# Performance work log

Measured on AMD Instinct MI355X. Metric: run time of the kernel, lower is better.

The kernel has to match this reference:

```python
import jax, jax.numpy as jnp
import numpy as np

C = 1024            # hidden_dim // compression_rate
IN_DIM = 1024
OUT_DIM = 1024
FFT_LEN = C // 2 + 1
CURV = 1e-4         # self.c
EPS = 1e-7
LN_EPS = 1e-5


def _mobius_scalar_mul(r, x, c):
    # r (x) x = tanh(r * atanh(sqrt(c)||x||)) * x / (sqrt(c)||x||)
    sqrt_c = jnp.sqrt(c)
    norm = jnp.maximum(jnp.linalg.norm(x, axis=-1, keepdims=True), EPS)
    scn = jnp.clip(sqrt_c * norm, EPS, 1.0 - 1e-5)
    return jnp.tanh(r * jnp.arctanh(scn)) * x / (sqrt_c * norm)


def _mobius_add(x, y, c):
    x2 = jnp.sum(x * x, axis=-1, keepdims=True)
    y2 = jnp.sum(y * y, axis=-1, keepdims=True)
    xy = jnp.sum(x * y, axis=-1, keepdims=True)
    num = (1.0 + 2.0 * c * xy + c * y2) * x + (1.0 - c * x2) * y
    den = 1.0 + 2.0 * c * xy + (c * c) * x2 * y2
    return num / jnp.maximum(den, EPS)


def _poincare_ball_layer(u, v, c, t):
    # geodesic-style interpolation: ((1-t) (x) u) (+) (t (x) v)
    return _mobius_add(_mobius_scalar_mul(1.0 - t, u, c),
                       _mobius_scalar_mul(t, v, c), c)


def setup_inputs() -> dict:
    key = jax.random.key(0)
    k_x, k_p, k_d = jax.random.split(key, 3)
    std = 0.02
    x = jax.random.normal(k_x, (4, 2048, IN_DIM), dtype=jnp.float32)
    proj_w = jax.random.normal(k_p, (C, IN_DIM), dtype=jnp.float32) * std
    freq_w = jnp.zeros((FFT_LEN,), dtype=jnp.float32)
    t = jnp.float32(0.3)
    ln_g = jnp.ones((C,), dtype=jnp.float32)
    ln_b = jnp.zeros((C,), dtype=jnp.float32)
    down_w = jax.random.normal(k_d, (OUT_DIM, C), dtype=jnp.float32) * std
    scale = jnp.float32(1.0)
    return {"x": x, "proj_w": proj_w, "ln_g": ln_g, "ln_b": ln_b,
            "freq_w": freq_w, "t": t, "down_w": down_w, "scale": scale}


def reference(x, proj_w, ln_g, ln_b, freq_w, t, down_w, scale):
    B, L, _ = x.shape
    # non-sep branch (hidden_dim > in_dim): silu(Linear(x))
    comp = jax.nn.silu(jnp.einsum('bli,ci->blc', x, proj_w))
    mu = jnp.mean(comp, axis=-1, keepdims=True)
    var = jnp.var(comp, axis=-1, keepdims=True)
    comp = (comp - mu) * jax.lax.rsqrt(var + LN_EPS) * ln_g + ln_b
    comp = comp.reshape(-1, C)                     # [B*L, C]
    Xf = jnp.fft.rfft(comp, axis=1)                # [B*L, C//2+1]
    w = jax.nn.softmax(freq_w)[None, :]
    flat = jnp.fft.irfft(Xf * w, n=C, axis=1)
    flat = jnp.nan_to_num(flat)
    shift = jnp.nan_to_num(t * flat)
    hyp = jnp.nan_to_num(_poincare_ball_layer(flat, shift, CURV, t))
    hyp = hyp.reshape(B, L, C)
    return jnp.einsum('blc,oc->blo', hyp, down_w) * scale
```

## Files before the change

### kernel.cpp

```cpp
#include <hip/hip_runtime.h>
#include <math.h>

typedef float f32x4 __attribute__((ext_vector_type(4)));
typedef __bf16 bf16x8 __attribute__((ext_vector_type(8)));

__device__ __forceinline__ unsigned short f2bf(float f) {
  unsigned u = __float_as_uint(f);
  unsigned r = (u + 0x7fffu + ((u >> 16) & 1u)) >> 16;
  return (unsigned short)r;
}
__device__ __forceinline__ float bf2f(unsigned short h) {
  return __uint_as_float(((unsigned)h) << 16);
}

__device__ __forceinline__ float blk_sum(float v, float* red, int tid) {
  #pragma unroll
  for (int o = 32; o; o >>= 1) v += __shfl_down(v, o);
  __syncthreads();
  if ((tid & 63) == 0) red[tid >> 6] = v;
  __syncthreads();
  return red[0] + red[1] + red[2] + red[3];
}

__global__ __launch_bounds__(256) void k_s(const float* __restrict__ fw,
                                           float* __restrict__ s) {
  __shared__ float wsh[513];
  __shared__ float red[4];
  int tid = threadIdx.x;
  float m = -1e30f;
  for (int i = tid; i < 513; i += 256) m = fmaxf(m, fw[i]);
  #pragma unroll
  for (int o = 32; o; o >>= 1) m = fmaxf(m, __shfl_down(m, o));
  if ((tid & 63) == 0) red[tid >> 6] = m;
  __syncthreads();
  m = fmaxf(fmaxf(red[0], red[1]), fmaxf(red[2], red[3]));
  float sum = 0.f;
  for (int i = tid; i < 513; i += 256) {
    float e = expf(fw[i] - m);
    wsh[i] = e;
    sum += e;
  }
  sum = blk_sum(sum, red, tid);
  float inv = 1.f / sum;

  int gid = blockIdx.x * 256 + tid;
  int d = gid >> 3;
  int chunk = gid & 7;
  float acc = 0.f;
  for (int f = 1 + chunk; f < 512; f += 8) {
    int p = (f * d) & 1023;
    acc += wsh[f] * __cosf(6.283185307179586f * (float)p * (1.f / 1024.f));
  }
  acc += __shfl_xor(acc, 1);
  acc += __shfl_xor(acc, 2);
  acc += __shfl_xor(acc, 4);
  if (chunk == 0) {
    float tot = wsh[0] + ((d & 1) ? -wsh[512] : wsh[512]) + 2.f * acc;
    s[d] = tot * inv * (1.f / 1024.f);
  }
}

__global__ __launch_bounds__(256) void k_prep(const float* __restrict__ x,
                                              const float* __restrict__ pw,
                                              const float* __restrict__ dw,
                                              const float* __restrict__ s,
                                              const float* __restrict__ ln_g,
                                              const float* __restrict__ ln_b,
                                              unsigned short* __restrict__ xb,
                                              unsigned short* __restrict__ pwb,
                                              unsigned short* __restrict__ dwb,
                                              unsigned short* __restrict__ Sg,
                                              float* __restrict__ Gs,
                                              float* __restrict__ Bs2) {
  __shared__ float red[4];
  int b = blockIdx.x;
  int tid = threadIdx.x;
  if (b < 8192) {
    int i = b * 256 + tid;
    float4 v = ((const float4*)x)[i];
    ushort4 o;
    o.x = f2bf(v.x); o.y = f2bf(v.y); o.z = f2bf(v.z); o.w = f2bf(v.w);
    ((ushort4*)xb)[i] = o;
  } else if (b < 9216) {
    int i = (b - 8192) * 256 + tid;
    float4 v = ((const float4*)pw)[i];
    ushort4 o;
    o.x = f2bf(v.x); o.y = f2bf(v.y); o.z = f2bf(v.z); o.w = f2bf(v.w);
    ((ushort4*)pwb)[i] = o;
  } else if (b < 10240) {
    int i = (b - 9216) * 256 + tid;
    float4 v = ((const float4*)dw)[i];
    ushort4 o;
    o.x = f2bf(v.x); o.y = f2bf(v.y); o.z = f2bf(v.z); o.w = f2bf(v.w);
    ((ushort4*)dwb)[i] = o;
  } else if (b < 11264) {
    int idx = (b - 10240) * 256 + tid;
    int n = idx >> 8;
    int k0 = (idx & 255) * 4;
    float4 gv = ((const float4*)ln_g)[idx & 255];
    ushort4 o;
    o.x = f2bf(gv.x * s[(k0 + 0 - n) & 1023]);
    o.y = f2bf(gv.y * s[(k0 + 1 - n) & 1023]);
    o.z = f2bf(gv.z * s[(k0 + 2 - n) & 1023]);
    o.w = f2bf(gv.w * s[(k0 + 3 - n) & 1023]);
    ((ushort4*)Sg)[idx] = o;
  } else {
    int n = b - 11264;
    int k0 = tid * 4;
    float4 gv = ((const float4*)ln_g)[tid];
    float4 bv = ((const float4*)ln_b)[tid];
    float s0 = s[(k0 + 0 - n) & 1023], s1 = s[(k0 + 1 - n) & 1023];
    float s2 = s[(k0 + 2 - n) & 1023], s3 = s[(k0 + 3 - n) & 1023];
    float gp = gv.x * s0 + gv.y * s1 + gv.z * s2 + gv.w * s3;
    float bp = bv.x * s0 + bv.y * s1 + bv.z * s2 + bv.w * s3;
    gp = blk_sum(gp, red, tid);
    bp = blk_sum(bp, red, tid);
    if (tid == 0) { Gs[n] = gp; Bs2[n] = bp; }
  }
}

__device__ __forceinline__ void gemm_body(const unsigned short* __restrict__ A,
                                          const unsigned short* __restrict__ B,
                                          int bm, int bn, int tid,
                                          char* AsB, char* BsB,
                                          f32x4 acc[4][4]) {
  const int lane = tid & 63;
  const int wave = tid >> 6;
  const int mhalf = (wave & 1) * 64;
  const int nhalf = (wave >> 1) * 64;
  const int ar = tid >> 3;
  const int ac = (((tid & 7) ^ (ar & 7))) * 8;
  const unsigned short* Abase = A + (size_t)(bm + ar) * 1024 + ac;
  const unsigned short* Bbase = B + (size_t)(bn + ar) * 1024 + ac;
  const int mrow = lane & 15;
  const int kq = lane >> 4;
  const int sw = mrow & 7;

  for (int kt = 0; kt < 16; ++kt) {
    const int k0 = kt * 64;
    #pragma unroll
    for (int r = 0; r < 4; ++r) {
      __builtin_amdgcn_global_load_lds(
          (const __attribute__((address_space(1))) void*)(Abase + (size_t)(r * 32) * 1024 + k0),
          (__attribute__((address_space(3))) void*)(AsB + r * 4096 + wave * 1024), 16, 0, 0);
      __builtin_amdgcn_global_load_lds(
          (const __attribute__((address_space(1))) void*)(Bbase + (size_t)(r * 32) * 1024 + k0),
          (__attribute__((address_space(3))) void*)(BsB + r * 4096 + wave * 1024), 16, 0, 0);
    }
    __syncthreads();
    #pragma unroll
    for (int kc = 0; kc < 2; ++kc) {
      const int chunk = (kc << 2) | kq;
      bf16x8 af[4], bfr[4];
      #pragma unroll
      for (int mt = 0; mt < 4; ++mt)
        af[mt] = *(const bf16x8*)(AsB + (mhalf + mt * 16 + mrow) * 128 + ((chunk ^ sw) << 4));
      #pragma unroll
      for (int nt = 0; nt < 4; ++nt)
        bfr[nt] = *(const bf16x8*)(BsB + (nhalf + nt * 16 + mrow) * 128 + ((chunk ^ sw) << 4));
      #pragma unroll
      for (int mt = 0; mt < 4; ++mt)
        #pragma unroll
        for (int nt = 0; nt < 4; ++nt)
          acc[mt][nt] = __builtin_amdgcn_mfma_f32_16x16x32_bf16(af[mt], bfr[nt], acc[mt][nt], 0, 0, 0);
    }
    __syncthreads();
  }
}

__global__ __launch_bounds__(256) void k_gemm1w2(const unsigned short* __restrict__ xb,
                                                 const unsigned short* __restrict__ pwb,
                                                 const unsigned short* __restrict__ dwb,
                                                 const unsigned short* __restrict__ Sg,
                                                 const float* __restrict__ ln_g,
                                                 const float* __restrict__ ln_b,
                                                 unsigned short* __restrict__ comp,
                                                 unsigned short* __restrict__ W2g,
                                                 float* __restrict__ rowsum,
                                                 float* __restrict__ rowsum2,
                                                 float* __restrict__ Gw,
                                                 float* __restrict__ Bw) {
  __shared__ __align__(16) unsigned short As[128 * 64];
  __shared__ __align__(16) unsigned short Bs[128 * 64];
  const int tid = threadIdx.x;
  const int lane = tid & 63;
  const int wave = tid >> 6;

  if (blockIdx.x < 256) {
    const unsigned short* Sc2 = Sg + (size_t)1024 * 1024;
    const int bm = ((int)blockIdx.x >> 4) * 64;
    const int bn = ((int)blockIdx.x & 15) * 64;
    const int wm = wave & 1;
    const int wn = wave >> 1;
    f32x4 acc[2][2] = {};
    const int ar = tid >> 3;
    const int ac = (((tid & 7) ^ (ar & 7))) * 8;
    const unsigned short* Abase = dwb + (size_t)(bm + ar) * 1024 + ac;
    const unsigned short* Bbase = Sc2 + (size_t)(bn + ar) * 1024 + ac;
    char* AsB = (char*)As;
    char* BsB = (char*)Bs;
    const int mrow = lane & 15;
    const int kq = lane >> 4;
    const int sw = mrow & 7;
    for (int kt = 0; kt < 16; ++kt) {
      const int k0 = kt * 64;
      #pragma unroll
      for (int r = 0; r < 2; ++r) {
        __builtin_amdgcn_global_load_lds(
            (const __attribute__((address_space(1))) void*)(Abase + (size_t)(r * 32) * 1024 + k0),
            (__attribute__((address_space(3))) void*)(AsB + r * 4096 + wave * 1024), 16, 0, 0);
        __builtin_amdgcn_global_load_lds(
            (const __attribute__((address_space(1))) void*)(Bbase + (size_t)(r * 32) * 1024 + k0),
            (__attribute__((address_space(3))) void*)(BsB + r * 4096 + wave * 1024), 16, 0, 0);
      }
      __syncthreads();
      #pragma unroll
      for (int kc = 0; kc < 2; ++kc) {
        const int chunk = (kc << 2) | kq;
        bf16x8 af[2], bfr[2];
        #pragma unroll
        for (int mt = 0; mt < 2; ++mt)
          af[mt] = *(const bf16x8*)(AsB + (wm * 32 + mt * 16 + mrow) * 128 + ((chunk ^ sw) << 4));
        #pragma unroll
        for (int nt = 0; nt < 2; ++nt)
          bfr[nt] = *(const bf16x8*)(BsB + (wn * 32 + nt * 16 + mrow) * 128 + ((chunk ^ sw) << 4));
        #pragma unroll
        for (int mt = 0; mt < 2; ++mt)
          #pragma unroll
          for (int nt = 0; nt < 2; ++nt)
            acc[mt][nt] = __builtin_amdgcn_mfma_f32_16x16x32_bf16(af[mt], bfr[nt], acc[mt][nt], 0, 0, 0);
      }
      __syncthreads();
    }
    const int col = bn + wn * 32 + (lane & 15);
    const int rbase = bm + wm * 32 + (lane >> 4) * 4;
    float gc[2], bc[2];
    #pragma unroll
    for (int nt = 0; nt < 2; ++nt) { gc[nt] = ln_g[col + nt * 16]; bc[nt] = ln_b[col + nt * 16]; }
    #pragma unroll
    for (int mt = 0; mt < 2; ++mt)
      #pragma unroll
      for (int r = 0; r < 4; ++r) {
        int row = rbase + mt * 16 + r;
        float gwp = 0.f, bwp = 0.f;
        #pragma unroll
        for (int nt = 0; nt < 2; ++nt) {
          float v = acc[mt][nt][r];
          W2g[(size_t)row * 1024 + (col + nt * 16)] = f2bf(gc[nt] * v);
          gwp += gc[nt] * v;
          bwp += bc[nt] * v;
        }
        gwp += __shfl_xor(gwp, 1); gwp += __shfl_xor(gwp, 2);
        gwp += __shfl_xor(gwp, 4); gwp += __shfl_xor(gwp, 8);
        bwp += __shfl_xor(bwp, 1); bwp += __shfl_xor(bwp, 2);
        bwp += __shfl_xor(bwp, 4); bwp += __shfl_xor(bwp, 8);
        if ((lane & 15) == 0) {
          atomicAdd(&Gw[row], gwp);
          atomicAdd(&Bw[row], bwp);
        }
      }
    return;
  }

  const int gid = blockIdx.x - 256;
  const int xcd = gid & 7;
  const int j = gid >> 3;
  const int ntile = j & 7;
  const int bmIdx = xcd + 8 * (j >> 3);
  const int bm = bmIdx * 128;
  const int bn = ntile * 128;
  f32x4 acc[4][4] = {};
  gemm_body(xb, pwb, bm, bn, tid, (char*)As, (char*)Bs, acc);

  const int col = bn + (wave >> 1) * 64 + (lane & 15);
  const int rbase = bm + (wave & 1) * 64 + (lane >> 4) * 4;
  #pragma unroll
  for (int mt = 0; mt < 4; ++mt)
    #pragma unroll
    for (int r = 0; r < 4; ++r) {
      const int row = rbase + mt * 16 + r;
      float s1 = 0.f, s2 = 0.f;
      #pragma unroll
      for (int nt = 0; nt < 4; ++nt) {
        float v = acc[mt][nt][r];
        float sv = v / (1.f + expf(-v));
        comp[(size_t)row * 1024 + (col + nt * 16)] = f2bf(sv);
        s1 += sv;
        s2 += sv * sv;
      }
      s1 += __shfl_xor(s1, 1); s1 += __shfl_xor(s1, 2);
      s1 += __shfl_xor(s1, 4); s1 += __shfl_xor(s1, 8);
      s2 += __shfl_xor(s2, 1); s2 += __shfl_xor(s2, 2);
      s2 += __shfl_xor(s2, 4); s2 += __shfl_xor(s2, 8);
      if ((lane & 15) == 0) {
        atomicAdd(&rowsum[row], s1);
        atomicAdd(&rowsum2[row], s2);
      }
    }
}

__device__ __forceinline__ float gamma_from_u2(float U2, float tv) {
  const float sc = 0.01f;
  const float c = 1e-4f;
  float nrm = sqrtf(U2);
  float nu = fmaxf(nrm, 1e-7f);
  float su = fminf(fmaxf(sc * nu, 1e-7f), 1.f - 1e-5f);
  float Af = tanhf((1.f - tv) * atanhf(su)) / (sc * nu);
  float nvn = fmaxf(fabsf(tv) * nrm, 1e-7f);
  float svv = fminf(fmaxf(sc * nvn, 1e-7f), 1.f - 1e-5f);
  float Bf = tv * tanhf(tv * atanhf(svv)) / (sc * nvn);
  float x2s = Af * Af * U2, y2s = Bf * Bf * U2, xys = Af * Bf * U2;
  float numc = (1.f + 2.f * c * xys + c * y2s) * Af + (1.f - c * x2s) * Bf;
  float den = fmaxf(1.f + 2.f * c * xys + c * c * x2s * y2s, 1e-7f);
  return numc / den;
}

__global__ __launch_bounds__(256) void k_gemm23(const unsigned short* __restrict__ comp,
                                                const unsigned short* __restrict__ Sg,
                                                const unsigned short* __restrict__ W2g,
                                                const float* __restrict__ rowsum,
                                                const float* __restrict__ rowsum2,
                                                const float* __restrict__ Gs,
                                                const float* __restrict__ Bs2,
                                                const float* __restrict__ Gw,
                                                const float* __restrict__ Bw,
                                                unsigned short* __restrict__ raw,
                                                float* __restrict__ u2) {
  __shared__ __align__(16) unsigned short As[128 * 64];
  __shared__ __align__(16) unsigned short Bs[128 * 64];
  __shared__ float muS[128], invS[128], GcS[128], BcS[128];
  const int tid = threadIdx.x;
  const int lane = tid & 63;
  const int wave = tid >> 6;
  const int xcd = blockIdx.x & 7;
  const int j = blockIdx.x >> 3;
  const int ntile = j & 15;
  const int bmIdx = xcd + 8 * (j >> 4);
  const int bm = bmIdx * 128;
  const bool isU2 = (ntile < 8);
  const int bn = (ntile & 7) * 128;
  const unsigned short* B = isU2 ? Sg : W2g;

  if (tid < 128) {
    float mu = rowsum[bm + tid] * (1.f / 1024.f);
    float ex2 = rowsum2[bm + tid] * (1.f / 1024.f);
    muS[tid] = mu;
    invS[tid] = rsqrtf(ex2 - mu * mu + 1e-5f);
  } else {
    int c = tid - 128;
    GcS[c] = isU2 ? Gs[bn + c] : Gw[bn + c];
    BcS[c] = isU2 ? Bs2[bn + c] : Bw[bn + c];
  }

  f32x4 acc[4][4] = {};
  gemm_body(comp, B, bm, bn, tid, (char*)As, (char*)Bs, acc);

  const int lcol = (wave >> 1) * 64 + (lane & 15);
  const int lrbase = (wave & 1) * 64 + (lane >> 4) * 4;
  #pragma unroll
  for (int mt = 0; mt < 4; ++mt)
    #pragma unroll
    for (int r = 0; r < 4; ++r) {
      const int lrow = lrbase + mt * 16 + r;
      const int row = bm + lrow;
      const float mu = muS[lrow];
      const float inv = invS[lrow];
      if (isU2) {
        float ssq = 0.f;
        #pragma unroll
        for (int nt = 0; nt < 4; ++nt) {
          int c = lcol + nt * 16;
          float v = inv * (acc[mt][nt][r] - mu * GcS[c]) + BcS[c];
          ssq += v * v;
        }
        ssq += __shfl_xor(ssq, 1);
        ssq += __shfl_xor(ssq, 2);
        ssq += __shfl_xor(ssq, 4);
        ssq += __shfl_xor(ssq, 8);
        if ((lane & 15) == 0) atomicAdd(&u2[row], ssq);
      } else {
        #pragma unroll
        for (int nt = 0; nt < 4; ++nt) {
          int c = lcol + nt * 16;
          float v = inv * (acc[mt][nt][r] - mu * GcS[c]) + BcS[c];
          raw[(size_t)row * 1024 + (bn + c)] = f2bf(v);
        }
      }
    }
}

__global__ __launch_bounds__(256) void k_out(const unsigned short* __restrict__ raw,
                                             const float* __restrict__ u2,
                                             const float* __restrict__ t_ptr,
                                             const float* __restrict__ scale_ptr,
                                             float* __restrict__ out) {
  __shared__ float gs;
  const int tid = threadIdx.x;
  const int row = blockIdx.x;
  if (tid == 0) gs = gamma_from_u2(u2[row], t_ptr[0]) * scale_ptr[0];
  __syncthreads();
  const float g = gs;
  ushort4 rv = ((const ushort4*)(raw + (size_t)row * 1024))[tid];
  float4 o;
  o.x = bf2f(rv.x) * g;
  o.y = bf2f(rv.y) * g;
  o.z = bf2f(rv.z) * g;
  o.w = bf2f(rv.w) * g;
  ((float4*)(out + (size_t)row * 1024))[tid] = o;
}

__global__ __launch_bounds__(256) void k_sc2(const float* __restrict__ s,
                                             unsigned short* __restrict__ Sc2) {
  int idx = blockIdx.x * 256 + threadIdx.x;
  int k = idx >> 8;
  int n0 = (idx & 255) * 4;
  ushort4 o;
  o.x = f2bf(s[(n0 + 0 - k) & 1023]);
  o.y = f2bf(s[(n0 + 1 - k) & 1023]);
  o.z = f2bf(s[(n0 + 2 - k) & 1023]);
  o.w = f2bf(s[(n0 + 3 - k) & 1023]);
  ((ushort4*)Sc2)[idx] = o;
}

extern "C" void kernel_launch(void* const* d_in, const int* in_sizes, int n_in,
                              void* d_out, int out_size, void* d_ws, size_t ws_size,
                              hipStream_t stream) {
  const float* x      = (const float*)d_in[0];
  const float* proj_w = (const float*)d_in[1];
  const float* ln_g   = (const float*)d_in[2];
  const float* ln_b   = (const float*)d_in[3];
  const float* freq_w = (const float*)d_in[4];
  const float* t_p    = (const float*)d_in[5];
  const float* down_w = (const float*)d_in[6];
  const float* scale  = (const float*)d_in[7];

  char* ws = (char*)d_ws;
  unsigned short* xb   = (unsigned short*)ws;
  unsigned short* pwb  = (unsigned short*)(ws + (16u << 20));
  unsigned short* dwb  = (unsigned short*)(ws + (18u << 20));
  unsigned short* comp = (unsigned short*)(ws + (20u << 20));
  unsigned short* Sg   = (unsigned short*)(ws + (36u << 20));
  unsigned short* Sc2  = (unsigned short*)(ws + (38u << 20));
  unsigned short* W2g  = (unsigned short*)(ws + (40u << 20));
  float* s_buf         = (float*)(ws + (42u << 20));
  float* stats         = (float*)(ws + (42u << 20) + 8192);
  float* rowsum  = stats;
  float* rowsum2 = stats + 8192;
  float* u2      = stats + 16384;
  float* Gw      = stats + 24576;
  float* Bw      = stats + 25600;
  float* Gs      = stats + 26624;
  float* Bs2     = stats + 27648;
  unsigned short* raw = xb;

  hipMemsetAsync(stats, 0, 28672 * sizeof(float), stream);
  k_s<<<32, 256, 0, stream>>>(freq_w, s_buf);
  k_prep<<<12288, 256, 0, stream>>>(x, proj_w, down_w, s_buf, ln_g, ln_b,
                                    xb, pwb, dwb, Sg, Gs, Bs2);
  k_sc2<<<1024, 256, 0, stream>>>(s_buf, Sc2);
  k_gemm1w2<<<768, 256, 0, stream>>>(xb, pwb, dwb, Sg, ln_g, ln_b,
                                     comp, W2g, rowsum, rowsum2, Gw, Bw);
  k_gemm23<<<1024, 256, 0, stream>>>(comp, Sg, W2g, rowsum, rowsum2,
                                     Gs, Bs2, Gw, Bw, raw, u2);
  k_out<<<8192, 256, 0, stream>>>(raw, u2, t_p, scale, (float*)d_out);
}
```

Baseline: 205.5 us.

## Retile first GEMM to 128x64, fold circulant build into prep, add occupancy hints

The x·proj_w GEMM moves from 128x128 tiles (512 blocks) to 128x64 tiles (1024 blocks), and its blocks now come before the small W2 blocks in the combined launch. The separate k_sc2 kernel is removed: k_prep now also writes the plain circulant matrix into a new Sb buffer. k_gemm23 drops its shared-memory staging of row stats and reads them straight from global memory. Both GEMM kernels get a launch_bounds occupancy hint of 5. The aim is to save one launch and to improve load balance and occupancy. The cost is lower per-tile data reuse in GEMM1 and repeated global reads of the stats in the epilogue. A __syncthreads is also added between the two block sums, which fixes a race on the shared reduction buffer.

```diff
diff --git a/kernel.cpp b/kernel.cpp
--- a/kernel.cpp
+++ b/kernel.cpp
@@ -69,6 +69,7 @@
                                               unsigned short* __restrict__ xb,
                                               unsigned short* __restrict__ pwb,
                                               unsigned short* __restrict__ dwb,
+                                              unsigned short* __restrict__ Sb,
                                               unsigned short* __restrict__ Sg,
                                               float* __restrict__ Gs,
                                               float* __restrict__ Bs2) {
@@ -97,6 +98,16 @@
     int idx = (b - 10240) * 256 + tid;
     int n = idx >> 8;
     int k0 = (idx & 255) * 4;
+    ushort4 o;
+    o.x = f2bf(s[(k0 + 0 - n) & 1023]);
+    o.y = f2bf(s[(k0 + 1 - n) & 1023]);
+    o.z = f2bf(s[(k0 + 2 - n) & 1023]);
+    o.w = f2bf(s[(k0 + 3 - n) & 1023]);
+    ((ushort4*)Sb)[idx] = o;
+  } else if (b < 12288) {
+    int idx = (b - 11264) * 256 + tid;
+    int n = idx >> 8;
+    int k0 = (idx & 255) * 4;
     float4 gv = ((const float4*)ln_g)[idx & 255];
     ushort4 o;
     o.x = f2bf(gv.x * s[(k0 + 0 - n) & 1023]);
@@ -105,7 +116,7 @@
     o.w = f2bf(gv.w * s[(k0 + 3 - n) & 1023]);
     ((ushort4*)Sg)[idx] = o;
   } else {
-    int n = b - 11264;
+    int n = b - 12288;
     int k0 = tid * 4;
     float4 gv = ((const float4*)ln_g)[tid];
     float4 bv = ((const float4*)ln_b)[tid];
@@ -114,6 +125,7 @@
     float gp = gv.x * s0 + gv.y * s1 + gv.z * s2 + gv.w * s3;
     float bp = bv.x * s0 + bv.y * s1 + bv.z * s2 + bv.w * s3;
     gp = blk_sum(gp, red, tid);
+    __syncthreads();
     bp = blk_sum(bp, red, tid);
     if (tid == 0) { Gs[n] = gp; Bs2[n] = bp; }
   }
@@ -168,133 +180,170 @@
   }
 }
 
-__global__ __launch_bounds__(256) void k_gemm1w2(const unsigned short* __restrict__ xb,
-                                                 const unsigned short* __restrict__ pwb,
-                                                 const unsigned short* __restrict__ dwb,
-                                                 const unsigned short* __restrict__ Sg,
-                                                 const float* __restrict__ ln_g,
-                                                 const float* __restrict__ ln_b,
-                                                 unsigned short* __restrict__ comp,
-                                                 unsigned short* __restrict__ W2g,
-                                                 float* __restrict__ rowsum,
-                                                 float* __restrict__ rowsum2,
-                                                 float* __restrict__ Gw,
-                                                 float* __restrict__ Bw) {
+__global__ __launch_bounds__(256, 5) void k_gemm1w2(const unsigned short* __restrict__ xb,
+                                                    const unsigned short* __restrict__ pwb,
+                                                    const unsigned short* __restrict__ dwb,
+                                                    const unsigned short* __restrict__ Sb,
+                                                    const float* __restrict__ ln_g,
+                                                    const float* __restrict__ ln_b,
+                                                    unsigned short* __restrict__ comp,
+                                                    unsigned short* __restrict__ W2g,
+                                                    float* __restrict__ rowsum,
+                                                    float* __restrict__ rowsum2,
+                                                    float* __restrict__ Gw,
+                                                    float* __restrict__ Bw) {
   __shared__ __align__(16) unsigned short As[128 * 64];
-  __shared__ __align__(16) unsigned short Bs[128 * 64];
+  __shared__ __align__(16) unsigned short Bs[64 * 64];
   const int tid = threadIdx.x;
   const int lane = tid & 63;
   const int wave = tid >> 6;
-
-  if (blockIdx.x < 256) {
-    const unsigned short* Sc2 = Sg + (size_t)1024 * 1024;
-    const int bm = ((int)blockIdx.x >> 4) * 64;
-    const int bn = ((int)blockIdx.x & 15) * 64;
-    const int wm = wave & 1;
-    const int wn = wave >> 1;
-    f32x4 acc[2][2] = {};
+  const int mrow = lane & 15;
+  const int kq = lane >> 4;
+  const int sw = mrow & 7;
+  char* AsB = (char*)As;
+  char* BsB = (char*)Bs;
+
+  if (blockIdx.x < 1024) {
+    const int gid = blockIdx.x;
+    const int xcd = gid & 7;
+    const int j = gid >> 3;
+    const int ntile = j & 15;
+    const int bmIdx = xcd + 8 * (j >> 4);
+    const int bm = bmIdx * 128;
+    const int bn = ntile * 64;
+    const int mhalf = (wave & 1) * 64;
+    const int nhalf = (wave >> 1) * 32;
+    f32x4 acc[4][2] = {};
     const int ar = tid >> 3;
     const int ac = (((tid & 7) ^ (ar & 7))) * 8;
-    const unsigned short* Abase = dwb + (size_t)(bm + ar) * 1024 + ac;
-    const unsigned short* Bbase = Sc2 + (size_t)(bn + ar) * 1024 + ac;
-    char* AsB = (char*)As;
-    char* BsB = (char*)Bs;
-    const int mrow = lane & 15;
-    const int kq = lane >> 4;
-    const int sw = mrow & 7;
+    const unsigned short* Abase = xb + (size_t)(bm + ar) * 1024 + ac;
+    const unsigned short* Bbase = pwb + (size_t)(bn + ar) * 1024 + ac;
+
     for (int kt = 0; kt < 16; ++kt) {
       const int k0 = kt * 64;
       #pragma unroll
-      for (int r = 0; r < 2; ++r) {
+      for (int r = 0; r < 4; ++r)
         __builtin_amdgcn_global_load_lds(
             (const __attribute__((address_space(1))) void*)(Abase + (size_t)(r * 32) * 1024 + k0),
             (__attribute__((address_space(3))) void*)(AsB + r * 4096 + wave * 1024), 16, 0, 0);
+      #pragma unroll
+      for (int r = 0; r < 2; ++r)
         __builtin_amdgcn_global_load_lds(
             (const __attribute__((address_space(1))) void*)(Bbase + (size_t)(r * 32) * 1024 + k0),
             (__attribute__((address_space(3))) void*)(BsB + r * 4096 + wave * 1024), 16, 0, 0);
-      }
       __syncthreads();
       #pragma unroll
       for (int kc = 0; kc < 2; ++kc) {
         const int chunk = (kc << 2) | kq;
-        bf16x8 af[2], bfr[2];
-        #pragma unroll
-        for (int mt = 0; mt < 2; ++mt)
-          af[mt] = *(const bf16x8*)(AsB + (wm * 32 + mt * 16 + mrow) * 128 + ((chunk ^ sw) << 4));
+        bf16x8 af[4], bfr[2];
+        #pragma unroll
+        for (int mt = 0; mt < 4; ++mt)
+          af[mt] = *(const bf16x8*)(AsB + (mhalf + mt * 16 + mrow) * 128 + ((chunk ^ sw) << 4));
         #pragma unroll
         for (int nt = 0; nt < 2; ++nt)
-          bfr[nt] = *(const bf16x8*)(BsB + (wn * 32 + nt * 16 + mrow) * 128 + ((chunk ^ sw) << 4));
-        #pragma unroll
-        for (int mt = 0; mt < 2; ++mt)
+          bfr[nt] = *(const bf16x8*)(BsB + (nhalf + nt * 16 + mrow) * 128 + ((chunk ^ sw) << 4));
+        #pragma unroll
+        for (int mt = 0; mt < 4; ++mt)
           #pragma unroll
           for (int nt = 0; nt < 2; ++nt)
             acc[mt][nt] = __builtin_amdgcn_mfma_f32_16x16x32_bf16(af[mt], bfr[nt], acc[mt][nt], 0, 0, 0);
       }
       __syncthreads();
     }
-    const int col = bn + wn * 32 + (lane & 15);
-    const int rbase = bm + wm * 32 + (lane >> 4) * 4;
-    float gc[2], bc[2];
-    #pragma unroll
-    for (int nt = 0; nt < 2; ++nt) { gc[nt] = ln_g[col + nt * 16]; bc[nt] = ln_b[col + nt * 16]; }
-    #pragma unroll
-    for (int mt = 0; mt < 2; ++mt)
+
+    const int col = bn + nhalf + (lane & 15);
+    const int rbase = bm + mhalf + (lane >> 4) * 4;
+    #pragma unroll
+    for (int mt = 0; mt < 4; ++mt)
       #pragma unroll
       for (int r = 0; r < 4; ++r) {
-        int row = rbase + mt * 16 + r;
-        float gwp = 0.f, bwp = 0.f;
+        const int row = rbase + mt * 16 + r;
+        float s1 = 0.f, s2 = 0.f;
         #pragma unroll
         for (int nt = 0; nt < 2; ++nt) {
           float v = acc[mt][nt][r];
-          W2g[(size_t)row * 1024 + (col + nt * 16)] = f2bf(gc[nt] * v);
-          gwp += gc[nt] * v;
-          bwp += bc[nt] * v;
+          float sv = v / (1.f + expf(-v));
+          comp[(size_t)row * 1024 + (col + nt * 16)] = f2bf(sv);
+          s1 += sv;
+          s2 += sv * sv;
         }
-        gwp += __shfl_xor(gwp, 1); gwp += __shfl_xor(gwp, 2);
-        gwp += __shfl_xor(gwp, 4); gwp += __shfl_xor(gwp, 8);
-        bwp += __shfl_xor(bwp, 1); bwp += __shfl_xor(bwp, 2);
-        bwp += __shfl_xor(bwp, 4); bwp += __shfl_xor(bwp, 8);
+        s1 += __shfl_xor(s1, 1); s1 += __shfl_xor(s1, 2);
+        s1 += __shfl_xor(s1, 4); s1 += __shfl_xor(s1, 8);
+        s2 += __shfl_xor(s2, 1); s2 += __shfl_xor(s2, 2);
+        s2 += __shfl_xor(s2, 4); s2 += __shfl_xor(s2, 8);
         if ((lane & 15) == 0) {
-          atomicAdd(&Gw[row], gwp);
-          atomicAdd(&Bw[row], bwp);
+          atomicAdd(&rowsum[row], s1);
+          atomicAdd(&rowsum2[row], s2);
         }
       }
     return;
   }
 
-  const int gid = blockIdx.x - 256;
-  const int xcd = gid & 7;
-  const int j = gid >> 3;
-  const int ntile = j & 7;
-  const int bmIdx = xcd + 8 * (j >> 3);
-  const int bm = bmIdx * 128;
-  const int bn = ntile * 128;
-  f32x4 acc[4][4] = {};
-  gemm_body(xb, pwb, bm, bn, tid, (char*)As, (char*)Bs, acc);
-
-  const int col = bn + (wave >> 1) * 64 + (lane & 15);
-  const int rbase = bm + (wave & 1) * 64 + (lane >> 4) * 4;
-  #pragma unroll
-  for (int mt = 0; mt < 4; ++mt)
+  const int wbid = blockIdx.x - 1024;
+  const int bm = (wbid >> 4) * 64;
+  const int bn = (wbid & 15) * 64;
+  const int wm = wave & 1;
+  const int wn = wave >> 1;
+  f32x4 acc[2][2] = {};
+  const int ar = tid >> 3;
+  const int ac = (((tid & 7) ^ (ar & 7))) * 8;
+  const unsigned short* Abase = dwb + (size_t)(bm + ar) * 1024 + ac;
+  const unsigned short* Bbase = Sb + (size_t)(bn + ar) * 1024 + ac;
+  for (int kt = 0; kt < 16; ++kt) {
+    const int k0 = kt * 64;
+    #pragma unroll
+    for (int r = 0; r < 2; ++r) {
+      __builtin_amdgcn_global_load_lds(
+          (const __attribute__((address_space(1))) void*)(Abase + (size_t)(r * 32) * 1024 + k0),
+          (__attribute__((address_space(3))) void*)(AsB + r * 4096 + wave * 1024), 16, 0, 0);
+      __builtin_amdgcn_global_load_lds(
+          (const __attribute__((address_space(1))) void*)(Bbase + (size_t)(r * 32) * 1024 + k0),
+          (__attribute__((address_space(3))) void*)(BsB + r * 4096 + wave * 1024), 16, 0, 0);
+    }
+    __syncthreads();
+    #pragma unroll
+    for (int kc = 0; kc < 2; ++kc) {
+      const int chunk = (kc << 2) | kq;
+      bf16x8 af[2], bfr[2];
+      #pragma unroll
+      for (int mt = 0; mt < 2; ++mt)
+        af[mt] = *(const bf16x8*)(AsB + (wm * 32 + mt * 16 + mrow) * 128 + ((chunk ^ sw) << 4));
+      #pragma unroll
+      for (int nt = 0; nt < 2; ++nt)
+        bfr[nt] = *(const bf16x8*)(BsB + (wn * 32 + nt * 16 + mrow) * 128 + ((chunk ^ sw) << 4));
+      #pragma unroll
+      for (int mt = 0; mt < 2; ++mt)
+        #pragma unroll
+        for (int nt = 0; nt < 2; ++nt)
+          acc[mt][nt] = __builtin_amdgcn_mfma_f32_16x16x32_bf16(af[mt], bfr[nt], acc[mt][nt], 0, 0, 0);
+    }
+    __syncthreads();
+  }
+  const int col = bn + wn * 32 + (lane & 15);
+  const int rbase = bm + wm * 32 + (lane >> 4) * 4;
+  float gc[2], bc[2];
+  #pragma unroll
+  for (int nt = 0; nt < 2; ++nt) { gc[nt] = ln_g[col + nt * 16]; bc[nt] = ln_b[col + nt * 16]; }
+  #pragma unroll
+  for (int mt = 0; mt < 2; ++mt)
     #pragma unroll
     for (int r = 0; r < 4; ++r) {
-      const int row = rbase + mt * 16 + r;
-      float s1 = 0.f, s2 = 0.f;
-      #pragma unroll
-      for (int nt = 0; nt < 4; ++nt) {
+      int row = rbase + mt * 16 + r;
+      float gwp = 0.f, bwp = 0.f;
+      #pragma unroll
+      for (int nt = 0; nt < 2; ++nt) {
         float v = acc[mt][nt][r];
-        float sv = v / (1.f + expf(-v));
-        comp[(size_t)row * 1024 + (col + nt * 16)] = f2bf(sv);
-        s1 += sv;
-        s2 += sv * sv;
+        W2g[(size_t)row * 1024 + (col + nt * 16)] = f2bf(gc[nt] * v);
+        gwp += gc[nt] * v;
+        bwp += bc[nt] * v;
       }
-      s1 += __shfl_xor(s1, 1); s1 += __shfl_xor(s1, 2);
-      s1 += __shfl_xor(s1, 4); s1 += __shfl_xor(s1, 8);
-      s2 += __shfl_xor(s2, 1); s2 += __shfl_xor(s2, 2);
-      s2 += __shfl_xor(s2, 4); s2 += __shfl_xor(s2, 8);
+      gwp += __shfl_xor(gwp, 1); gwp += __shfl_xor(gwp, 2);
+      gwp += __shfl_xor(gwp, 4); gwp += __shfl_xor(gwp, 8);
+      bwp += __shfl_xor(bwp, 1); bwp += __shfl_xor(bwp, 2);
+      bwp += __shfl_xor(bwp, 4); bwp += __shfl_xor(bwp, 8);
       if ((lane & 15) == 0) {
-        atomicAdd(&rowsum[row], s1);
-        atomicAdd(&rowsum2[row], s2);
+        atomicAdd(&Gw[row], gwp);
+        atomicAdd(&Bw[row], bwp);
       }
     }
 }
@@ -315,20 +364,19 @@
   return numc / den;
 }
 
-__global__ __launch_bounds__(256) void k_gemm23(const unsigned short* __restrict__ comp,
-                                                const unsigned short* __restrict__ Sg,
-                                                const unsigned short* __restrict__ W2g,
-                                                const float* __restrict__ rowsum,
-                                                const float* __restrict__ rowsum2,
-                                                const float* __restrict__ Gs,
-                                                const float* __restrict__ Bs2,
-                                                const float* __restrict__ Gw,
-                                                const float* __restrict__ Bw,
-                                                unsigned short* __restrict__ raw,
-                                                float* __restrict__ u2) {
+__global__ __launch_bounds__(256, 5) void k_gemm23(const unsigned short* __restrict__ comp,
+                                                   const unsigned short* __restrict__ Sg,
+                                                   const unsigned short* __restrict__ W2g,
+                                                   const float* __restrict__ rowsum,
+                                                   const float* __restrict__ rowsum2,
+                                                   const float* __restrict__ Gs,
+                                                   const float* __restrict__ Bs2,
+                                                   const float* __restrict__ Gw,
+                                                   const float* __restrict__ Bw,
+                                                   unsigned short* __restrict__ raw,
+                                                   float* __restrict__ u2) {
   __shared__ __align__(16) unsigned short As[128 * 64];
   __shared__ __align__(16) unsigned short Bs[128 * 64];
-  __shared__ float muS[128], invS[128], GcS[128], BcS[128];
   const int tid = threadIdx.x;
   const int lane = tid & 63;
   const int wave = tid >> 6;
@@ -340,37 +388,31 @@
   const bool isU2 = (ntile < 8);
   const int bn = (ntile & 7) * 128;
   const unsigned short* B = isU2 ? Sg : W2g;
-
-  if (tid < 128) {
-    float mu = rowsum[bm + tid] * (1.f / 1024.f);
-    float ex2 = rowsum2[bm + tid] * (1.f / 1024.f);
-    muS[tid] = mu;
-    invS[tid] = rsqrtf(ex2 - mu * mu + 1e-5f);
-  } else {
-    int c = tid - 128;
-    GcS[c] = isU2 ? Gs[bn + c] : Gw[bn + c];
-    BcS[c] = isU2 ? Bs2[bn + c] : Bw[bn + c];
-  }
-
   f32x4 acc[4][4] = {};
   gemm_body(comp, B, bm, bn, tid, (char*)As, (char*)Bs, acc);
 
-  const int lcol = (wave >> 1) * 64 + (lane & 15);
-  const int lrbase = (wave & 1) * 64 + (lane >> 4) * 4;
+  const int col = bn + (wave >> 1) * 64 + (lane & 15);
+  const int rbase = bm + (wave & 1) * 64 + (lane >> 4) * 4;
+  const float* Gp = isU2 ? Gs : Gw;
+  const float* Bp = isU2 ? Bs2 : Bw;
+  float Gc[4], Bc[4];
+  #pragma unroll
+  for (int nt = 0; nt < 4; ++nt) {
+    Gc[nt] = Gp[col + nt * 16];
+    Bc[nt] = Bp[col + nt * 16];
+  }
   #pragma unroll
   for (int mt = 0; mt < 4; ++mt)
     #pragma unroll
     for (int r = 0; r < 4; ++r) {
-      const int lrow = lrbase + mt * 16 + r;
-      const int row = bm + lrow;
-      const float mu = muS[lrow];
-      const float inv = invS[lrow];
+      const int row = rbase + mt * 16 + r;
+      float mu = rowsum[row] * (1.f / 1024.f);
+      float inv = rsqrtf(rowsum2[row] * (1.f / 1024.f) - mu * mu + 1e-5f);
       if (isU2) {
         float ssq = 0.f;
         #pragma unroll
         for (int nt = 0; nt < 4; ++nt) {
-          int c = lcol + nt * 16;
-          float v = inv * (acc[mt][nt][r] - mu * GcS[c]) + BcS[c];
+          float v = inv * (acc[mt][nt][r] - mu * Gc[nt]) + Bc[nt];
           ssq += v * v;
         }
         ssq += __shfl_xor(ssq, 1);
@@ -381,9 +423,8 @@
       } else {
         #pragma unroll
         for (int nt = 0; nt < 4; ++nt) {
-          int c = lcol + nt * 16;
-          float v = inv * (acc[mt][nt][r] - mu * GcS[c]) + BcS[c];
-          raw[(size_t)row * 1024 + (bn + c)] = f2bf(v);
+          float v = inv * (acc[mt][nt][r] - mu * Gc[nt]) + Bc[nt];
+          raw[(size_t)row * 1024 + (col + nt * 16)] = f2bf(v);
         }
       }
     }
@@ -409,19 +450,6 @@
   ((float4*)(out + (size_t)row * 1024))[tid] = o;
 }
 
-__global__ __launch_bounds__(256) void k_sc2(const float* __restrict__ s,
-                                             unsigned short* __restrict__ Sc2) {
-  int idx = blockIdx.x * 256 + threadIdx.x;
-  int k = idx >> 8;
-  int n0 = (idx & 255) * 4;
-  ushort4 o;
-  o.x = f2bf(s[(n0 + 0 - k) & 1023]);
-  o.y = f2bf(s[(n0 + 1 - k) & 1023]);
-  o.z = f2bf(s[(n0 + 2 - k) & 1023]);
-  o.w = f2bf(s[(n0 + 3 - k) & 1023]);
-  ((ushort4*)Sc2)[idx] = o;
-}
-
 extern "C" void kernel_launch(void* const* d_in, const int* in_sizes, int n_in,
                               void* d_out, int out_size, void* d_ws, size_t ws_size,
                               hipStream_t stream) {
@@ -439,8 +467,8 @@
   unsigned short* pwb  = (unsigned short*)(ws + (16u << 20));
   unsigned short* dwb  = (unsigned short*)(ws + (18u << 20));
   unsigned short* comp = (unsigned short*)(ws + (20u << 20));
-  unsigned short* Sg   = (unsigned short*)(ws + (36u << 20));
-  unsigned short* Sc2  = (unsigned short*)(ws + (38u << 20));
+  unsigned short* Sb   = (unsigned short*)(ws + (36u << 20));
+  unsigned short* Sg   = (unsigned short*)(ws + (38u << 20));
   unsigned short* W2g  = (unsigned short*)(ws + (40u << 20));
   float* s_buf         = (float*)(ws + (42u << 20));
   float* stats         = (float*)(ws + (42u << 20) + 8192);
@@ -453,13 +481,12 @@
   float* Bs2     = stats + 27648;
   unsigned short* raw = xb;
 
-  hipMemsetAsync(stats, 0, 28672 * sizeof(float), stream);
+  hipMemsetAsync(stats, 0, 26624 * sizeof(float), stream);
   k_s<<<32, 256, 0, stream>>>(freq_w, s_buf);
-  k_prep<<<12288, 256, 0, stream>>>(x, proj_w, down_w, s_buf, ln_g, ln_b,
-                                    xb, pwb, dwb, Sg, Gs, Bs2);
-  k_sc2<<<1024, 256, 0, stream>>>(s_buf, Sc2);
-  k_gemm1w2<<<768, 256, 0, stream>>>(xb, pwb, dwb, Sg, ln_g, ln_b,
-                                     comp, W2g, rowsum, rowsum2, Gw, Bw);
+  k_prep<<<13312, 256, 0, stream>>>(x, proj_w, down_w, s_buf, ln_g, ln_b,
+                                    xb, pwb, dwb, Sb, Sg, Gs, Bs2);
+  k_gemm1w2<<<1280, 256, 0, stream>>>(xb, pwb, dwb, Sb, ln_g, ln_b,
+                                      comp, W2g, rowsum, rowsum2, Gw, Bw);
   k_gemm23<<<1024, 256, 0, stream>>>(comp, Sg, W2g, rowsum, rowsum2,
                                      Gs, Bs2, Gw, Bw, raw, u2);
   k_out<<<8192, 256, 0, stream>>>(raw, u2, t_p, scale, (float*)d_out);
```

Result: faster. 199.8 us (-2.8%).
